# Performance work log

Hardware: AMD Instinct MI355X
Metric: run time of the kernel (lower is better)

Reference implementation:

```python
import jax, jax.numpy as jnp
import numpy as np

N = 10000   # nodes
B = 32      # batch (hardcoded in source)
E = 40000   # edges per graph
H = 4       # attention heads
D = 10      # out_feats per head (hardcoded 10 in source)
T = 10      # GAT input feature size (hardcoded 10)
L = 2       # n_align_layers
NEG = 0.2   # LeakyReLU slope


def _leaky(z):
    return jnp.where(z >= 0, z, NEG * z)


def _ln(t):
    # LayerNorm((N,B,D), elementwise_affine=False): normalize over the whole tensor
    m = t.mean()
    v = ((t - m) ** 2).mean()
    return (t - m) * jax.lax.rsqrt(v + 1e-5)


def _gat(feat, fc_w, a_l, a_r, src, dst):
    # feat: (N,B,T); fc_w: (H*D,T); a_l,a_r: (H,D); src,dst: (E,)
    ft = jnp.einsum('nbf,of->nbo', feat, fc_w).reshape(N, B, H, D)
    el = jnp.einsum('nbhd,hd->nbh', ft, a_l)   # (N,B,H)
    er = jnp.einsum('nbhd,hd->nbh', ft, a_r)
    e = _leaky(el[src] + er[dst])              # (E,B,H)
    emax = jax.ops.segment_max(e, dst, num_segments=N)
    ee = jnp.exp(e - emax[dst])
    a = ee / jax.ops.segment_sum(ee, dst, num_segments=N)[dst]  # edge softmax per dst
    out = jax.ops.segment_sum(ft[src] * a[..., None], dst, num_segments=N)  # (N,B,H,D)
    return _leaky(out)  # activation = leaky_relu in source


def setup_inputs():
    key = jax.random.key(0)
    ks = iter(jax.random.split(key, 40))
    x = jax.random.normal(next(ks), (T, N, B, 3), dtype=jnp.float32)
    idx = lambda: jax.random.randint(next(ks), (E,), 0, N, dtype=jnp.int32)
    inp = {'x': x, 'ps_src': idx(), 'ps_dst': idx(), 'rl_src': idx(), 'rl_dst': idx()}
    def gat_params(name):
        inp[name + '_fc'] = jax.random.normal(next(ks), (L, H * D, T), dtype=jnp.float32) * 0.3
        inp[name + '_al'] = jax.random.normal(next(ks), (L, H, D), dtype=jnp.float32) * 0.3
        inp[name + '_ar'] = jax.random.normal(next(ks), (L, H, D), dtype=jnp.float32) * 0.3
    for nm in ('mu_p', 'sg_p', 'mu_r', 'sg_r'):
        gat_params(nm)
    inp['reg_mu_w'] = jax.random.normal(next(ks), (1, T), dtype=jnp.float32) * 0.3
    inp['reg_mu_b'] = jnp.zeros((1,), dtype=jnp.float32)
    inp['reg_sg_w'] = jax.random.normal(next(ks), (1, T), dtype=jnp.float32) * 0.3
    inp['reg_sg_b'] = jnp.zeros((1,), dtype=jnp.float32)
    return inp


def reference(x, mu_p_fc, mu_p_al, mu_p_ar, sg_p_fc, sg_p_al, sg_p_ar,
              mu_r_fc, mu_r_al, mu_r_ar, sg_r_fc, sg_r_al, sg_r_ar,
              reg_mu_w, reg_mu_b, reg_sg_w, reg_sg_b,
              ps_src, ps_dst, rl_src, rl_dst):
    # mode='align1' path of Net.forward
    h = jnp.transpose(x, (1, 2, 0, 3))[..., :3]  # (N,B,T,3)
    mu = h[..., 0]      # (N,B,T)
    sigma = h[..., 1]
    mu_r0, sg_r0 = mu, sigma
    # pseudo-graph alignment stack
    mu_p, sg_p = mu, sigma
    for i in range(L - 1):
        mu_p = _ln(_gat(mu_p, mu_p_fc[i], mu_p_al[i], mu_p_ar[i], ps_src, ps_dst).mean(-2))
        sg_p = _ln(_gat(sg_p, sg_p_fc[i], sg_p_al[i], sg_p_ar[i], ps_src, ps_dst).mean(-2))
        h_p = (mu_p + sg_p) / 2
        mu_p, sg_p = h_p, h_p
    # real-graph alignment stack
    mu_rl, sg_rl = mu, sigma
    for i in range(L - 1):
        mu_rl = _ln(_gat(mu_rl, mu_r_fc[i], mu_r_al[i], mu_r_ar[i], rl_src, rl_dst).mean(-2))
        sg_rl = _ln(_gat(sg_rl, sg_r_fc[i], sg_r_al[i], sg_r_ar[i], rl_src, rl_dst).mean(-2))
        h_rl = (mu_rl + sg_rl) / 2
        mu_rl, sg_rl = h_rl, h_rl
    mu_r = mu_r0 @ reg_mu_w.T + reg_mu_b                                        # (N,B,1)
    mu_pf = _gat(h_p, mu_p_fc[-1], mu_p_al[-1], mu_p_ar[-1], ps_src, ps_dst).mean(-2)
    mu_rf = _gat(h_rl, mu_r_fc[-1], mu_r_al[-1], mu_r_ar[-1], rl_src, rl_dst).mean(-2)
    sg_r = sg_r0 @ reg_sg_w.T + reg_sg_b
    sg_pf = _gat(h_p, sg_p_fc[-1], sg_p_al[-1], sg_p_ar[-1], ps_src, ps_dst).mean(-2)
    sg_rf = _gat(h_rl, sg_r_fc[-1], sg_r_al[-1], sg_r_ar[-1], rl_src, rl_dst).mean(-2)
    return ((mu_r + mu_pf + mu_rf) / 3, (sg_r + sg_pf + sg_rf) / 3)
```

## Files before the change

kernel.cpp:

```cpp
#include <hip/hip_runtime.h>

#define NN 10000
#define BB 32
#define EE 40000
#define HH 4
#define DD 10
#define TT 10
#define FS 12
#define MS 24
#define NEG 0.2f

#define NB   (NN*BB)
#define NBT  (NN*BB*TT)
#define NBF  (NN*BB*FS)
#define NBM  (NN*BB*MS)

__global__ void extract_kernel(const float* __restrict__ x,
                               const float* __restrict__ wmu, const float* __restrict__ bmu,
                               const float* __restrict__ wsg, const float* __restrict__ bsg,
                               float* __restrict__ ms,
                               float* __restrict__ regmu, float* __restrict__ regsg) {
    int i = blockIdx.x * blockDim.x + threadIdx.x;
    if (i >= NB) return;
    int n = i / BB, b = i % BB;
    float smu = 0.f, ssg = 0.f;
    float muv[TT], sgv[TT];
#pragma unroll
    for (int t = 0; t < TT; t++) {
        size_t xi = (((size_t)t * NN + n) * BB + b) * 3;
        float m = x[xi], s = x[xi + 1];
        muv[t] = m; sgv[t] = s;
        smu += m * wmu[t];
        ssg += s * wsg[t];
    }
#pragma unroll
    for (int t = 0; t < TT; t++) {
        ms[(size_t)i * MS + t]      = muv[t];
        ms[(size_t)i * MS + 12 + t] = sgv[t];
    }
    regmu[i] = smu + bmu[0];
    regsg[i] = ssg + bsg[0];
}

__global__ void deg2_kernel(const int* __restrict__ dst0, int* __restrict__ deg0,
                            const int* __restrict__ dst1, int* __restrict__ deg1) {
    int e = blockIdx.x * blockDim.x + threadIdx.x;
    const int* dst = blockIdx.y ? dst1 : dst0;
    int* deg       = blockIdx.y ? deg1 : deg0;
    if (e < EE) atomicAdd(&deg[dst[e]], 1);
}

__global__ void scan2_kernel(const int* __restrict__ deg0, int* __restrict__ off0,
                             const int* __restrict__ deg1, int* __restrict__ off1) {
    const int* __restrict__ deg = blockIdx.x ? deg1 : deg0;
    int* __restrict__ off       = blockIdx.x ? off1 : off0;
    __shared__ int sm[16];
    __shared__ int carry_s;
    int tid = threadIdx.x;
    int lane = tid & 63, wid = tid >> 6;
    if (tid == 0) { carry_s = 0; off[0] = 0; }
    __syncthreads();
    for (int base = 0; base < NN; base += 1024) {
        int i = base + tid;
        int v = (i < NN) ? deg[i] : 0;
        int x = v;
#pragma unroll
        for (int s = 1; s < 64; s <<= 1) {
            int t = __shfl_up(x, s, 64);
            if (lane >= s) x += t;
        }
        if (lane == 63) sm[wid] = x;
        __syncthreads();
        if (wid == 0) {
            int w = (lane < 16) ? sm[lane] : 0;
#pragma unroll
            for (int s = 1; s < 16; s <<= 1) {
                int t = __shfl_up(w, s, 64);
                if (lane >= s) w += t;
            }
            if (lane < 16) sm[lane] = w;
        }
        __syncthreads();
        int add = carry_s + ((wid > 0) ? sm[wid - 1] : 0);
        if (i < NN) off[i + 1] = add + x;
        int total = sm[15];
        __syncthreads();
        if (tid == 0) carry_s += total;
        __syncthreads();
    }
}

__global__ void fill2_kernel(const int* __restrict__ src0, const int* __restrict__ dst0,
                             const int* __restrict__ off0, int* __restrict__ cur0,
                             int* __restrict__ csr0,
                             const int* __restrict__ src1, const int* __restrict__ dst1,
                             const int* __restrict__ off1, int* __restrict__ cur1,
                             int* __restrict__ csr1) {
    int e = blockIdx.x * blockDim.x + threadIdx.x;
    const int* src = blockIdx.y ? src1 : src0;
    const int* dst = blockIdx.y ? dst1 : dst0;
    const int* off = blockIdx.y ? off1 : off0;
    int* cursor    = blockIdx.y ? cur1 : cur0;
    int* csr       = blockIdx.y ? csr1 : csr0;
    if (e < EE) {
        int d = dst[e];
        int p = atomicAdd(&cursor[d], 1);
        csr[off[d] + p] = src[e];
    }
}

__global__ void vpre_kernel(const float* __restrict__ fc0, const float* __restrict__ al0, const float* __restrict__ ar0,
                            const float* __restrict__ fc1, const float* __restrict__ al1, const float* __restrict__ ar1,
                            const float* __restrict__ fc2, const float* __restrict__ al2, const float* __restrict__ ar2,
                            const float* __restrict__ fc3, const float* __restrict__ al3, const float* __restrict__ ar3,
                            float* __restrict__ vbuf) {
    int j = threadIdx.x;
    if (j >= 320) return;
    int g = j / 40, r = j % 40;
    int h = r / 10, t = r % 10;
    int which = g & 3, layer = g >> 2;
    const float* fc; const float* al; const float* ar;
    if (which == 0)      { fc = fc0; al = al0; ar = ar0; }
    else if (which == 1) { fc = fc1; al = al1; ar = ar1; }
    else if (which == 2) { fc = fc2; al = al2; ar = ar2; }
    else                 { fc = fc3; al = al3; ar = ar3; }
    fc += layer * (HH * DD * TT);
    al += layer * (HH * DD);
    ar += layer * (HH * DD);
    float vl = 0.f, vr = 0.f;
#pragma unroll
    for (int d = 0; d < DD; d++) {
        float w = fc[(h * DD + d) * TT + t];
        vl += al[h * DD + d] * w;
        vr += ar[h * DD + d] * w;
    }
    vbuf[g * 80 + r] = vl;
    vbuf[g * 80 + 40 + r] = vr;
}

struct PairCfg {
    const float* f;
    const float* WA; const float* WB;
    const float* vA; const float* vB;
    const int* off; const int* csr;
    float* gA; float* gB;
    float* statsA; float* statsB;
};
struct PairCfg2 { PairCfg c[2]; };

#define LOAD_ROW(dst, q)                                        \
    {                                                           \
        float4 _r0 = *(const float4*)(q);                       \
        float4 _r1 = *(const float4*)((q) + 4);                 \
        float2 _r2 = *(const float2*)((q) + 8);                 \
        dst[0]=_r0.x; dst[1]=_r0.y; dst[2]=_r0.z; dst[3]=_r0.w; \
        dst[4]=_r1.x; dst[5]=_r1.y; dst[6]=_r1.z; dst[7]=_r1.w; \
        dst[8]=_r2.x; dst[9]=_r2.y;                             \
    }

__device__ __forceinline__ void eacc(const float (&fa)[TT], bool val,
                                     const float* __restrict__ v,
                                     const float (&er)[HH],
                                     float (&den)[HH], float (&acc)[HH][TT]) {
#pragma unroll
    for (int h = 0; h < HH; h++) {
        float e = 0.f;
#pragma unroll
        for (int t = 0; t < TT; t++) e += v[h * TT + t] * fa[t];
        float z = e + er[h];
        z = (z >= 0.f) ? z : NEG * z;
        float w = val ? __expf(z) : 0.f;
        den[h] += w;
#pragma unroll
        for (int t = 0; t < TT; t++) acc[h][t] += w * fa[t];
    }
}

template <bool DUALF, bool STATS>
__global__ void __launch_bounds__(256)
gatpair_kernel(PairCfg2 cfgs) {
    const PairCfg cfg = cfgs.c[blockIdx.y];
    __shared__ __align__(16) float sWA[HH * DD * 12];
    __shared__ __align__(16) float sWB[HH * DD * 12];
    for (int kk = threadIdx.x; kk < HH * DD * TT; kk += blockDim.x) {
        int r = kk / TT, t = kk - r * TT;
        sWA[r * 12 + t] = cfg.WA[kk];
        sWB[r * 12 + t] = cfg.WB[kk];
    }
    __syncthreads();

    const float* __restrict__ f   = cfg.f;
    const int*   __restrict__ csr = cfg.csr;
    const float* __restrict__ vA  = cfg.vA;
    const float* __restrict__ vB  = cfg.vB;
    const int LDR = DUALF ? MS : FS;

    int i = blockIdx.x * blockDim.x + threadIdx.x;
    float lsA = 0.f, lqA = 0.f, lsB = 0.f, lqB = 0.f;
    if (i < NB) {
        int b = i & 31;
        int n = i >> 5;
        int s0 = cfg.off[n], s1 = cfg.off[n + 1];

        float erA[HH], erB[HH];
        {
            const float* p = f + (size_t)i * LDR;
            float fsA[TT];
            LOAD_ROW(fsA, p);
            float fsB[TT];
            if (DUALF) { LOAD_ROW(fsB, p + 12); }
#pragma unroll
            for (int h = 0; h < HH; h++) {
                float ea = 0.f, eb = 0.f;
#pragma unroll
                for (int t = 0; t < TT; t++) {
                    ea += vA[HH * TT + h * TT + t] * fsA[t];
                    eb += vB[HH * TT + h * TT + t] * (DUALF ? fsB[t] : fsA[t]);
                }
                erA[h] = ea; erB[h] = eb;
            }
        }

        float accA[HH][TT], accB[HH][TT];
        float denA[HH], denB[HH];
#pragma unroll
        for (int h = 0; h < HH; h++) {
            denA[h] = 0.f; denB[h] = 0.f;
#pragma unroll
            for (int t = 0; t < TT; t++) { accA[h][t] = 0.f; accB[h][t] = 0.f; }
        }

        for (int k = s0; k < s1; k += 2) {
            int k1 = (k + 1 < s1) ? k + 1 : k;
            bool v1 = (k + 1 < s1);
            int e0 = csr[k], e1 = csr[k1];
            const float* q0 = f + (size_t)(e0 * BB + b) * LDR;
            const float* q1 = f + (size_t)(e1 * BB + b) * LDR;
            float a0[TT], a1[TT];
            LOAD_ROW(a0, q0);
            LOAD_ROW(a1, q1);
            if (DUALF) {
                float b0[TT], b1[TT];
                LOAD_ROW(b0, q0 + 12);
                LOAD_ROW(b1, q1 + 12);
                eacc(a0, true, vA, erA, denA, accA);
                eacc(b0, true, vB, erB, denB, accB);
                eacc(a1, v1,   vA, erA, denA, accA);
                eacc(b1, v1,   vB, erB, denB, accB);
            } else {
                eacc(a0, true, vA, erA, denA, accA);
                eacc(a0, true, vB, erB, denB, accB);
                eacc(a1, v1,   vA, erA, denA, accA);
                eacc(a1, v1,   vB, erB, denB, accB);
            }
        }

        bool nz = (s1 > s0);
        float* gpA = cfg.gA + (size_t)i * DD;
        float* gpB = cfg.gB + (size_t)i * DD;

#pragma unroll
        for (int g = 0; g < 2; g++) {
            const float (*acc)[TT] = g ? accB : accA;
            const float* den = g ? denB : denA;
            const float* sW  = g ? sWB : sWA;
            float* gp        = g ? gpB : gpA;
            float rd[HH];
#pragma unroll
            for (int h = 0; h < HH; h++) rd[h] = nz ? (1.0f / den[h]) : 0.f;
            float outv[DD];
#pragma unroll
            for (int d = 0; d < DD; d++) outv[d] = 0.f;
#pragma unroll
            for (int h = 0; h < HH; h++) {
#pragma unroll
                for (int d = 0; d < DD; d++) {
                    const float* wr = &sW[(h * DD + d) * 12];
                    float4 w0 = *(const float4*)wr;
                    float4 w1 = *(const float4*)(wr + 4);
                    float2 w2 = *(const float2*)(wr + 8);
                    float va = w0.x * acc[h][0] + w0.y * acc[h][1] + w0.z * acc[h][2] + w0.w * acc[h][3]
                             + w1.x * acc[h][4] + w1.y * acc[h][5] + w1.z * acc[h][6] + w1.w * acc[h][7]
                             + w2.x * acc[h][8] + w2.y * acc[h][9];
                    va *= rd[h];
                    va = (va >= 0.f) ? va : NEG * va;
                    outv[d] += va * 0.25f;
                }
            }
#pragma unroll
            for (int d = 0; d < DD; d += 2)
                *(float2*)(gp + d) = make_float2(outv[d], outv[d + 1]);
            if (STATS) {
                float s = 0.f, q = 0.f;
#pragma unroll
                for (int d = 0; d < DD; d++) { s += outv[d]; q += outv[d] * outv[d]; }
                if (g) { lsB = s; lqB = q; } else { lsA = s; lqA = q; }
            }
        }
    }
    if (STATS) {
#pragma unroll
        for (int o = 32; o > 0; o >>= 1) {
            lsA += __shfl_down(lsA, o, 64);
            lqA += __shfl_down(lqA, o, 64);
            lsB += __shfl_down(lsB, o, 64);
            lqB += __shfl_down(lqB, o, 64);
        }
        __shared__ float ss[4][4];
        int wid = threadIdx.x >> 6, lid = threadIdx.x & 63;
        if (lid == 0) { ss[wid][0] = lsA; ss[wid][1] = lqA; ss[wid][2] = lsB; ss[wid][3] = lqB; }
        __syncthreads();
        if (threadIdx.x == 0) {
            float a0 = 0.f, a1 = 0.f, a2 = 0.f, a3 = 0.f;
#pragma unroll
            for (int w = 0; w < 4; w++) { a0 += ss[w][0]; a1 += ss[w][1]; a2 += ss[w][2]; a3 += ss[w][3]; }
            atomicAdd(&cfg.statsA[0], a0);
            atomicAdd(&cfg.statsA[1], a1);
            atomicAdd(&cfg.statsB[0], a2);
            atomicAdd(&cfg.statsB[1], a3);
        }
    }
}

__global__ void lncomb2_kernel(const float* __restrict__ gA, const float* __restrict__ gB,
                               const float* __restrict__ gA2, const float* __restrict__ gB2,
                               const float* __restrict__ stats,
                               float* __restrict__ hp, float* __restrict__ hrl) {
    int i = blockIdx.x * blockDim.x + threadIdx.x;
    if (i >= NBT) return;
    const float* ga = blockIdx.y ? gA2 : gA;
    const float* gb = blockIdx.y ? gB2 : gB;
    const float* st = stats + (blockIdx.y ? 4 : 0);
    float* h        = blockIdx.y ? hrl : hp;
    const float M = (float)NBT;
    float ma = st[0] / M; float va = st[1] / M - ma * ma;
    float mb = st[2] / M; float vb = st[3] / M - mb * mb;
    float ra = rsqrtf(va + 1e-5f), rb = rsqrtf(vb + 1e-5f);
    int nb = i / DD, t = i - nb * DD;
    h[(size_t)nb * FS + t] = 0.5f * ((ga[i] - ma) * ra + (gb[i] - mb) * rb);
}

__global__ void outcomb2_kernel(const float* __restrict__ regmu, const float* __restrict__ regsg,
                                const float* __restrict__ gA, const float* __restrict__ gA2,
                                const float* __restrict__ gB, const float* __restrict__ gB2,
                                float* __restrict__ out) {
    int i = blockIdx.x * blockDim.x + threadIdx.x;
    if (i >= NBT) return;
    int nb = i / DD;
    if (blockIdx.y == 0) out[i]       = (regmu[nb] + gA[i] + gA2[i]) * (1.0f / 3.0f);
    else                 out[NBT + i] = (regsg[nb] + gB[i] + gB2[i]) * (1.0f / 3.0f);
}

extern "C" void kernel_launch(void* const* d_in, const int* in_sizes, int n_in,
                              void* d_out, int out_size, void* d_ws, size_t ws_size,
                              hipStream_t stream) {
    const float* x      = (const float*)d_in[0];
    const int* ps_src   = (const int*)d_in[1];
    const int* ps_dst   = (const int*)d_in[2];
    const int* rl_src   = (const int*)d_in[3];
    const int* rl_dst   = (const int*)d_in[4];
    const float* mu_p_fc = (const float*)d_in[5];
    const float* mu_p_al = (const float*)d_in[6];
    const float* mu_p_ar = (const float*)d_in[7];
    const float* sg_p_fc = (const float*)d_in[8];
    const float* sg_p_al = (const float*)d_in[9];
    const float* sg_p_ar = (const float*)d_in[10];
    const float* mu_r_fc = (const float*)d_in[11];
    const float* mu_r_al = (const float*)d_in[12];
    const float* mu_r_ar = (const float*)d_in[13];
    const float* sg_r_fc = (const float*)d_in[14];
    const float* sg_r_al = (const float*)d_in[15];
    const float* sg_r_ar = (const float*)d_in[16];
    const float* reg_mu_w = (const float*)d_in[17];
    const float* reg_mu_b = (const float*)d_in[18];
    const float* reg_sg_w = (const float*)d_in[19];
    const float* reg_sg_b = (const float*)d_in[20];

    float* out = (float*)d_out;

    float* fw = (float*)d_ws;
    float* ms    = fw;              fw += NBM;
    float* hp    = fw;              fw += NBF;
    float* hrl   = fw;              fw += NBF;
    float* gA    = fw;              fw += NBT;
    float* gB    = fw;              fw += NBT;
    float* gA2   = fw;              fw += NBT;
    float* gB2   = fw;              fw += NBT;
    float* regmu = fw;              fw += NB;
    float* regsg = fw;              fw += NB;
    float* vbuf  = fw;              fw += 8 * 80;
    int* iw = (int*)fw;
    int* ps_off = iw;               iw += NN + 1;
    int* rl_off = iw;               iw += NN + 1;
    int* ps_csr = iw;               iw += EE;
    int* rl_csr = iw;               iw += EE;
    int* deg_ps = iw;               iw += NN;
    int* cur_ps = iw;               iw += NN;
    int* deg_rl = iw;               iw += NN;
    int* cur_rl = iw;               iw += NN;
    float* stats = (float*)iw;
    size_t zero_bytes = (size_t)(4 * NN) * sizeof(int) + 8 * sizeof(float);
    hipMemsetAsync(deg_ps, 0, zero_bytes, stream);

    const int TPB = 256;
    const int GRID_NB  = (NB + TPB - 1) / TPB;
    const int GRID_NBT = (NBT + TPB - 1) / TPB;
    const int GRID_E   = (EE + TPB - 1) / TPB;

    extract_kernel<<<GRID_NB, TPB, 0, stream>>>(x, reg_mu_w, reg_mu_b, reg_sg_w, reg_sg_b,
                                                ms, regmu, regsg);

    {
        dim3 g(GRID_E, 2, 1);
        deg2_kernel<<<g, TPB, 0, stream>>>(ps_dst, deg_ps, rl_dst, deg_rl);
        scan2_kernel<<<2, 1024, 0, stream>>>(deg_ps, ps_off, deg_rl, rl_off);
        fill2_kernel<<<g, TPB, 0, stream>>>(ps_src, ps_dst, ps_off, cur_ps, ps_csr,
                                            rl_src, rl_dst, rl_off, cur_rl, rl_csr);
    }

    vpre_kernel<<<1, 320, 0, stream>>>(mu_p_fc, mu_p_al, mu_p_ar,
                                       sg_p_fc, sg_p_al, sg_p_ar,
                                       mu_r_fc, mu_r_al, mu_r_ar,
                                       sg_r_fc, sg_r_al, sg_r_ar, vbuf);

    {
        PairCfg2 c;
        c.c[0] = { ms, mu_p_fc, sg_p_fc, vbuf + 0 * 80, vbuf + 1 * 80,
                   ps_off, ps_csr, gA,  gB,  stats + 0, stats + 2 };
        c.c[1] = { ms, mu_r_fc, sg_r_fc, vbuf + 2 * 80, vbuf + 3 * 80,
                   rl_off, rl_csr, gA2, gB2, stats + 4, stats + 6 };
        dim3 grid(GRID_NB, 2, 1);
        gatpair_kernel<true, true><<<grid, TPB, 0, stream>>>(c);
    }
    {
        dim3 g(GRID_NBT, 2, 1);
        lncomb2_kernel<<<g, TPB, 0, stream>>>(gA, gB, gA2, gB2, stats, hp, hrl);
    }

    {
        PairCfg2 c;
        c.c[0] = { hp,  mu_p_fc + 400, sg_p_fc + 400, vbuf + 4 * 80, vbuf + 5 * 80,
                   ps_off, ps_csr, gA,  gB,  nullptr, nullptr };
        c.c[1] = { hrl, mu_r_fc + 400, sg_r_fc + 400, vbuf + 6 * 80, vbuf + 7 * 80,
                   rl_off, rl_csr, gA2, gB2, nullptr, nullptr };
        dim3 grid(GRID_NB, 2, 1);
        gatpair_kernel<false, false><<<grid, TPB, 0, stream>>>(c);
    }

    {
        dim3 g(GRID_NBT, 2, 1);
        outcomb2_kernel<<<g, TPB, 0, stream>>>(regmu, regsg, gA, gA2, gB, gB2, out);
    }
}
```

Baseline: 420.4 us.

## Sort destination nodes by in-degree to balance GAT aggregation warps

Adds a counting-sort pass (histogram, scan, permutation fill) that orders nodes by descending in-degree, clamped at 63. The GAT pair kernels then map each 32-lane batch group to a permuted node. Wavefronts of 64 lanes cover two nodes, so pairing nodes of similar degree cuts divergence, since each wave runs for the maximum degree of its nodes. It adds three small kernels and an extra indirection, and output writes become scattered at node granularity.

Result: no change. 413.2 us (-1.7%).

```diff
diff --git a/kernel.cpp b/kernel.cpp
--- a/kernel.cpp
+++ b/kernel.cpp
@@ -1,4 +1,5 @@
 #include <hip/hip_runtime.h>
+
 
 #define NN 10000
 #define BB 32
@@ -107,6 +108,61 @@
         int p = atomicAdd(&cursor[d], 1);
         csr[off[d] + p] = src[e];
     }
+}
+
+__global__ void hist2_kernel(const int* __restrict__ deg0, const int* __restrict__ deg1,
+                             int* __restrict__ hist) {
+    __shared__ int lh[64];
+    if (threadIdx.x < 64) lh[threadIdx.x] = 0;
+    __syncthreads();
+    int n = blockIdx.x * blockDim.x + threadIdx.x;
+    int g = blockIdx.y;
+    const int* deg = g ? deg1 : deg0;
+    if (n < NN) {
+        int d = deg[n];
+        int bin = 63 - ((d < 63) ? d : 63);
+        atomicAdd(&lh[bin], 1);
+    }
+    __syncthreads();
+    if (threadIdx.x < 64 && lh[threadIdx.x])
+        atomicAdd(&hist[g * 64 + threadIdx.x], lh[threadIdx.x]);
+}
+
+__global__ void binoff_kernel(const int* __restrict__ hist, int* __restrict__ boff) {
+    int g = threadIdx.x >> 6, lane = threadIdx.x & 63;
+    int v = hist[g * 64 + lane];
+    int x = v;
+#pragma unroll
+    for (int s = 1; s < 64; s <<= 1) {
+        int t = __shfl_up(x, s, 64);
+        if (lane >= s) x += t;
+    }
+    boff[g * 64 + lane] = x - v;
+}
+
+__global__ void permfill2_kernel(const int* __restrict__ deg0, const int* __restrict__ deg1,
+                                 const int* __restrict__ boff, int* __restrict__ bcur,
+                                 int* __restrict__ perm0, int* __restrict__ perm1) {
+    __shared__ int lh[64], lbase[64];
+    if (threadIdx.x < 64) lh[threadIdx.x] = 0;
+    __syncthreads();
+    int n = blockIdx.x * blockDim.x + threadIdx.x;
+    int g = blockIdx.y;
+    const int* deg = g ? deg1 : deg0;
+    int* perm      = g ? perm1 : perm0;
+    int bin = 0, myp = 0;
+    if (n < NN) {
+        int d = deg[n];
+        bin = 63 - ((d < 63) ? d : 63);
+        myp = atomicAdd(&lh[bin], 1);
+    }
+    __syncthreads();
+    if (threadIdx.x < 64) {
+        int c = lh[threadIdx.x];
+        lbase[threadIdx.x] = c ? atomicAdd(&bcur[g * 64 + threadIdx.x], c) : 0;
+    }
+    __syncthreads();
+    if (n < NN) perm[boff[g * 64 + bin] + lbase[bin] + myp] = n;
 }
 
 __global__ void vpre_kernel(const float* __restrict__ fc0, const float* __restrict__ al0, const float* __restrict__ ar0,
@@ -142,7 +198,7 @@
     const float* f;
     const float* WA; const float* WB;
     const float* vA; const float* vB;
-    const int* off; const int* csr;
+    const int* off; const int* csr; const int* perm;
     float* gA; float* gB;
     float* statsA; float* statsB;
 };
@@ -199,12 +255,14 @@
     float lsA = 0.f, lqA = 0.f, lsB = 0.f, lqB = 0.f;
     if (i < NB) {
         int b = i & 31;
-        int n = i >> 5;
+        int slot = i >> 5;
+        int n = cfg.perm[slot];
+        int nb = n * BB + b;
         int s0 = cfg.off[n], s1 = cfg.off[n + 1];
 
         float erA[HH], erB[HH];
         {
-            const float* p = f + (size_t)i * LDR;
+            const float* p = f + (size_t)nb * LDR;
             float fsA[TT];
             LOAD_ROW(fsA, p);
             float fsB[TT];
@@ -256,8 +314,8 @@
         }
 
         bool nz = (s1 > s0);
-        float* gpA = cfg.gA + (size_t)i * DD;
-        float* gpB = cfg.gB + (size_t)i * DD;
+        float* gpA = cfg.gA + (size_t)nb * DD;
+        float* gpB = cfg.gB + (size_t)nb * DD;
 
 #pragma unroll
         for (int g = 0; g < 2; g++) {
@@ -394,28 +452,38 @@
     int* rl_off = iw;               iw += NN + 1;
     int* ps_csr = iw;               iw += EE;
     int* rl_csr = iw;               iw += EE;
+    int* perm_ps = iw;              iw += NN;
+    int* perm_rl = iw;              iw += NN;
+    int* boff   = iw;               iw += 128;
     int* deg_ps = iw;               iw += NN;
     int* cur_ps = iw;               iw += NN;
     int* deg_rl = iw;               iw += NN;
     int* cur_rl = iw;               iw += NN;
+    int* hist   = iw;               iw += 128;
+    int* bcur   = iw;               iw += 128;
     float* stats = (float*)iw;
-    size_t zero_bytes = (size_t)(4 * NN) * sizeof(int) + 8 * sizeof(float);
+    size_t zero_bytes = (size_t)(4 * NN + 256) * sizeof(int) + 8 * sizeof(float);
     hipMemsetAsync(deg_ps, 0, zero_bytes, stream);
 
     const int TPB = 256;
     const int GRID_NB  = (NB + TPB - 1) / TPB;
     const int GRID_NBT = (NBT + TPB - 1) / TPB;
     const int GRID_E   = (EE + TPB - 1) / TPB;
+    const int GRID_N   = (NN + TPB - 1) / TPB;
 
     extract_kernel<<<GRID_NB, TPB, 0, stream>>>(x, reg_mu_w, reg_mu_b, reg_sg_w, reg_sg_b,
                                                 ms, regmu, regsg);
 
     {
         dim3 g(GRID_E, 2, 1);
+        dim3 gn(GRID_N, 2, 1);
         deg2_kernel<<<g, TPB, 0, stream>>>(ps_dst, deg_ps, rl_dst, deg_rl);
         scan2_kernel<<<2, 1024, 0, stream>>>(deg_ps, ps_off, deg_rl, rl_off);
         fill2_kernel<<<g, TPB, 0, stream>>>(ps_src, ps_dst, ps_off, cur_ps, ps_csr,
                                             rl_src, rl_dst, rl_off, cur_rl, rl_csr);
+        hist2_kernel<<<gn, TPB, 0, stream>>>(deg_ps, deg_rl, hist);
+        binoff_kernel<<<1, 128, 0, stream>>>(hist, boff);
+        permfill2_kernel<<<gn, TPB, 0, stream>>>(deg_ps, deg_rl, boff, bcur, perm_ps, perm_rl);
     }
 
     vpre_kernel<<<1, 320, 0, stream>>>(mu_p_fc, mu_p_al, mu_p_ar,
@@ -426,9 +494,9 @@
     {
         PairCfg2 c;
         c.c[0] = { ms, mu_p_fc, sg_p_fc, vbuf + 0 * 80, vbuf + 1 * 80,
-                   ps_off, ps_csr, gA,  gB,  stats + 0, stats + 2 };
+                   ps_off, ps_csr, perm_ps, gA,  gB,  stats + 0, stats + 2 };
         c.c[1] = { ms, mu_r_fc, sg_r_fc, vbuf + 2 * 80, vbuf + 3 * 80,
-                   rl_off, rl_csr, gA2, gB2, stats + 4, stats + 6 };
+                   rl_off, rl_csr, perm_rl, gA2, gB2, stats + 4, stats + 6 };
         dim3 grid(GRID_NB, 2, 1);
         gatpair_kernel<true, true><<<grid, TPB, 0, stream>>>(c);
     }
@@ -440,9 +508,9 @@
     {
         PairCfg2 c;
         c.c[0] = { hp,  mu_p_fc + 400, sg_p_fc + 400, vbuf + 4 * 80, vbuf + 5 * 80,
-                   ps_off, ps_csr, gA,  gB,  nullptr, nullptr };
+                   ps_off, ps_csr, perm_ps, gA,  gB,  nullptr, nullptr };
         c.c[1] = { hrl, mu_r_fc + 400, sg_r_fc + 400, vbuf + 6 * 80, vbuf + 7 * 80,
-                   rl_off, rl_csr, gA2, gB2, nullptr, nullptr };
+                   rl_off, rl_csr, perm_rl, gA2, gB2, nullptr, nullptr };
         dim3 grid(GRID_NB, 2, 1);
         gatpair_kernel<false, false><<<grid, TPB, 0, stream>>>(c);
     }
```
